# Performance work log

Measured on AMD Instinct MI355X. Metric: run time of the kernel, lower is better.

Reference implementation:

```python
import jax, jax.numpy as jnp
import numpy as np

N_NODES = 100000
N_EDGES = 1600000
IN_DIM, HID_DIM, OUT_DIM = 128, 64, 40


def gcn_conv(x, src, dst, deg_inv_sqrt, W, b):
    # PyG GCNConv: out[dst] += norm(e) * (x @ W)[src] ; norm = d^-1/2[src]*d^-1/2[dst]
    h = x @ W                                   # [N, out]
    norm = deg_inv_sqrt[src] * deg_inv_sqrt[dst]  # [E]
    msgs = h[src] * norm[:, None]               # [E, out] gather
    out = jax.ops.segment_sum(msgs, dst, num_segments=x.shape[0])  # scatter-add
    return out + b


def setup_inputs() -> dict:
    key = jax.random.key(0)
    k1, k2, k3, k4, k5, k6 = jax.random.split(key, 6)
    x = jax.random.normal(k1, (N_NODES, IN_DIM), dtype=jnp.float32)
    edge_index = jax.random.randint(k2, (2, N_EDGES), 0, N_NODES, dtype=jnp.int64)
    # Glorot-style init for linear weights, zero bias (as in GCNConv defaults)
    W1 = jax.random.normal(k3, (IN_DIM, HID_DIM), dtype=jnp.float32) / np.sqrt(IN_DIM)
    b1 = jnp.zeros((HID_DIM,), dtype=jnp.float32)
    W2 = jax.random.normal(k4, (HID_DIM, OUT_DIM), dtype=jnp.float32) / np.sqrt(HID_DIM)
    b2 = jnp.zeros((OUT_DIM,), dtype=jnp.float32)
    return {"x": x, "edge_index": edge_index, "W1": W1, "b1": b1, "W2": W2, "b2": b2}


def reference(x, edge_index, W1, b1, W2, b2):
    N = x.shape[0]
    loop = jnp.arange(N, dtype=edge_index.dtype)
    src = jnp.concatenate([edge_index[0], loop])  # add self-loops
    dst = jnp.concatenate([edge_index[1], loop])
    # symmetric normalization: degree over destination (col) with unit edge weights
    deg = jax.ops.segment_sum(jnp.ones_like(dst, dtype=x.dtype), dst, num_segments=N)
    deg_inv_sqrt = jnp.where(deg > 0, jax.lax.rsqrt(deg), 0.0)

    h = jax.nn.relu(gcn_conv(x, src, dst, deg_inv_sqrt, W1, b1))
    h = gcn_conv(h, src, dst, deg_inv_sqrt, W2, b2)
    return jax.nn.log_softmax(h, axis=1)
```

## Files before the change

### kernel.cpp

```cpp
#include <hip/hip_runtime.h>
#include <hip/hip_bf16.h>
#include <math.h>

typedef long long i64;
typedef __attribute__((ext_vector_type(8))) short short8v;
typedef __attribute__((ext_vector_type(4))) float f32x4;

__device__ __forceinline__ float bfu(unsigned short u) {
    union { unsigned int i; float f; } v; v.i = ((unsigned)u) << 16; return v.f;
}
__device__ __forceinline__ unsigned short f2b(float f) {
    __hip_bfloat16 h = __float2bfloat16(f);
    return *reinterpret_cast<unsigned short*>(&h);
}

#define NPB_SHIFT 9
#define NPB 512
#define LCAP 16384
#define P1C 8192

__global__ void k_zeroB(int* __restrict__ bcnt, int B) {
    int t = threadIdx.x;
    if (t <= B) bcnt[t] = 0;
}

__global__ __launch_bounds__(256) void k_p1count(
    const int* __restrict__ dst, int E, int B, int* __restrict__ bcnt) {
    __shared__ int lb[256];
    int t = threadIdx.x;
    lb[t] = 0; __syncthreads();
    int cpb = (E + gridDim.x - 1) / gridDim.x;
    int s0 = blockIdx.x * cpb, s1 = min(E, s0 + cpb);
    for (int i = s0 + t; i < s1; i += 256)
        atomicAdd(&lb[dst[i] >> NPB_SHIFT], 1);
    __syncthreads();
    if (t < B && lb[t]) atomicAdd(&bcnt[t], lb[t]);
}

__global__ void k_scanB(const int* __restrict__ bcnt, int B, int E,
                        int* __restrict__ bstart, int* __restrict__ cursor) {
    __shared__ int s[256];
    int t = threadIdx.x;
    int v = (t < B) ? bcnt[t] : 0;
    s[t] = v; __syncthreads();
    for (int off = 1; off < 256; off <<= 1) {
        int u = (t >= off) ? s[t - off] : 0;
        __syncthreads();
        s[t] += u;
        __syncthreads();
    }
    int excl = s[t] - v;
    if (t < B) { bstart[t] = excl; cursor[t] = excl; }
    if (t == 0) bstart[B] = E;
}

__global__ __launch_bounds__(256) void k_p1place(
    const int* __restrict__ src, const int* __restrict__ dst, int E, int B,
    int* __restrict__ cursor, unsigned* __restrict__ pairs) {
    __shared__ unsigned ls_p[P1C];
    __shared__ unsigned char ls_b[P1C];
    __shared__ int lb[256];
    __shared__ int lbase[256];
    int t = threadIdx.x;
    int s0 = blockIdx.x * P1C, s1 = min(E, s0 + P1C), n = s1 - s0;
    lb[t] = 0; __syncthreads();
    for (int i = t; i < n; i += 256) {
        int d = dst[s0 + i];
        int s = src[s0 + i];
        int bkt = d >> NPB_SHIFT;
        ls_p[i] = (unsigned)s | ((unsigned)(d & (NPB - 1)) << 17);
        ls_b[i] = (unsigned char)bkt;
        atomicAdd(&lb[bkt], 1);
    }
    __syncthreads();
    if (t < B && lb[t]) lbase[t] = atomicAdd(&cursor[t], lb[t]);
    __syncthreads();
    lb[t] = 0; __syncthreads();
    for (int i = t; i < n; i += 256) {
        int bkt = ls_b[i];
        int slot = atomicAdd(&lb[bkt], 1);
        pairs[lbase[bkt] + slot] = ls_p[i];
    }
}

__global__ __launch_bounds__(512) void k_p2(
    const unsigned* __restrict__ pairs, const int* __restrict__ bstart,
    int* __restrict__ rowptr, float* __restrict__ dinv,
    int* __restrict__ col, int N, int E) {
    __shared__ int lcnt[NPB];
    __shared__ int lscan[NPB];
    __shared__ int lcol[LCAP];
    int b = blockIdx.x, t = threadIdx.x;
    int lo = b << NPB_SHIFT, hi = min(N, lo + NPB), nn = hi - lo;
    int e0 = bstart[b], e1 = bstart[b + 1];
    lcnt[t] = 0; __syncthreads();
    for (int i = e0 + t; i < e1; i += 512)
        atomicAdd(&lcnt[(int)(pairs[i] >> 17)], 1);
    __syncthreads();
    int myc = (t < nn) ? lcnt[t] : 0;
    lscan[t] = myc; __syncthreads();
    for (int off = 1; off < 512; off <<= 1) {
        int u = (t >= off) ? lscan[t - off] : 0;
        __syncthreads();
        lscan[t] += u;
        __syncthreads();
    }
    if (t < nn) {
        rowptr[lo + t] = e0 + lscan[t] - myc;
        dinv[lo + t] = rsqrtf((float)(myc + 1));
    }
    if (t == 0 && hi == N) rowptr[N] = E;
    __syncthreads();
    lscan[t] -= myc;
    lcnt[t] = 0;
    __syncthreads();
    for (int i = e0 + t; i < e1; i += 512) {
        unsigned p = pairs[i];
        int n = (int)(p >> 17);
        int slot = atomicAdd(&lcnt[n], 1);
        int idx = lscan[n] + slot;
        if (idx < LCAP) lcol[idx] = (int)(p & 0x1FFFFu);
    }
    __syncthreads();
    int cnt = e1 - e0;
    for (int i = t; i < cnt; i += 512) col[e0 + i] = lcol[i];
}


__global__ __launch_bounds__(256) void k_gemm1m(
    const float* __restrict__ X, const float* __restrict__ W,
    const float* __restrict__ dinv, unsigned short* __restrict__ out, int N) {
    __shared__ unsigned short Xs[128 * 128];
    __shared__ unsigned short Wt[64 * 128];
    int tid = threadIdx.x;
    int row0 = blockIdx.x << 7;

    for (int i = tid; i < 2048; i += 256) {
        float4 v = *(const float4*)(W + i * 4);
        int k = (i * 4) >> 6, n = (i * 4) & 63;
        int kb = k * 2;
        *(unsigned short*)((char*)Wt + (n + 0) * 256 + (kb ^ (((n + 0) & 7) << 4))) = f2b(v.x);
        *(unsigned short*)((char*)Wt + (n + 1) * 256 + (kb ^ (((n + 1) & 7) << 4))) = f2b(v.y);
        *(unsigned short*)((char*)Wt + (n + 2) * 256 + (kb ^ (((n + 2) & 7) << 4))) = f2b(v.z);
        *(unsigned short*)((char*)Wt + (n + 3) * 256 + (kb ^ (((n + 3) & 7) << 4))) = f2b(v.w);
    }
    for (int i = tid; i < 4096; i += 256) {
        int r = i >> 5, c4 = i & 31;
        int gr = row0 + r;
        float4 v = make_float4(0.f, 0.f, 0.f, 0.f);
        if (gr < N) v = *(const float4*)(X + (size_t)gr * 128 + c4 * 4);
        ushort4 h;
        h.x = f2b(v.x); h.y = f2b(v.y); h.z = f2b(v.z); h.w = f2b(v.w);
        *(ushort4*)((char*)Xs + r * 256 + ((c4 * 8) ^ ((r & 7) << 4))) = h;
    }
    __syncthreads();

    int wid = tid >> 6, lane = tid & 63;
    int l15 = lane & 15, lg = lane >> 4;
    int wrow = wid * 32;

    f32x4 acc[2][4];
    #pragma unroll
    for (int fr = 0; fr < 2; fr++)
        #pragma unroll
        for (int fc = 0; fc < 4; fc++) acc[fr][fc] = (f32x4){0.f, 0.f, 0.f, 0.f};

    #pragma unroll
    for (int ks = 0; ks < 4; ks++) {
        int kbyte = ks * 64 + lg * 16;
        int ra0 = wrow + l15, ra1 = wrow + 16 + l15;
        short8v a0 = *(short8v*)((char*)Xs + ra0 * 256 + (kbyte ^ ((ra0 & 7) << 4)));
        short8v a1 = *(short8v*)((char*)Xs + ra1 * 256 + (kbyte ^ ((ra1 & 7) << 4)));
        int swb = kbyte ^ ((l15 & 7) << 4);
        short8v b0 = *(short8v*)((char*)Wt + (l15) * 256 + swb);
        short8v b1 = *(short8v*)((char*)Wt + (16 + l15) * 256 + swb);
        short8v b2 = *(short8v*)((char*)Wt + (32 + l15) * 256 + swb);
        short8v b3 = *(short8v*)((char*)Wt + (48 + l15) * 256 + swb);
        acc[0][0] = __builtin_amdgcn_mfma_f32_16x16x32_bf16(a0, b0, acc[0][0], 0, 0, 0);
        acc[0][1] = __builtin_amdgcn_mfma_f32_16x16x32_bf16(a0, b1, acc[0][1], 0, 0, 0);
        acc[0][2] = __builtin_amdgcn_mfma_f32_16x16x32_bf16(a0, b2, acc[0][2], 0, 0, 0);
        acc[0][3] = __builtin_amdgcn_mfma_f32_16x16x32_bf16(a0, b3, acc[0][3], 0, 0, 0);
        acc[1][0] = __builtin_amdgcn_mfma_f32_16x16x32_bf16(a1, b0, acc[1][0], 0, 0, 0);
        acc[1][1] = __builtin_amdgcn_mfma_f32_16x16x32_bf16(a1, b1, acc[1][1], 0, 0, 0);
        acc[1][2] = __builtin_amdgcn_mfma_f32_16x16x32_bf16(a1, b2, acc[1][2], 0, 0, 0);
        acc[1][3] = __builtin_amdgcn_mfma_f32_16x16x32_bf16(a1, b3, acc[1][3], 0, 0, 0);
    }

    float dv[2][4];
    #pragma unroll
    for (int fr = 0; fr < 2; fr++)
        #pragma unroll
        for (int reg = 0; reg < 4; reg++) {
            int grow = row0 + wrow + fr * 16 + lg * 4 + reg;
            dv[fr][reg] = (grow < N) ? dinv[grow] : 0.f;
        }
    #pragma unroll
    for (int fr = 0; fr < 2; fr++)
        #pragma unroll
        for (int fc = 0; fc < 4; fc++)
            #pragma unroll
            for (int reg = 0; reg < 4; reg++) {
                int grow = row0 + wrow + fr * 16 + lg * 4 + reg;
                if (grow < N)
                    out[(size_t)grow * 64 + fc * 16 + l15] = f2b(acc[fr][fc][reg] * dv[fr][reg]);
            }
}


template<bool L1>
__global__ __launch_bounds__(256) void k_agg(
    const unsigned short* __restrict__ gsrc, const int* __restrict__ rowptr,
    const int* __restrict__ col, const float* __restrict__ dinv,
    const float* __restrict__ b1, unsigned short* __restrict__ gout, int N) {
    int gw = (int)((blockIdx.x * 256u + threadIdx.x) >> 6);
    int lane = threadIdx.x & 63;
    int li = lane & 31;
    int node = gw * 2 + (lane >> 5);
    bool valid = node < N;
    int r0 = 0, r1 = 0;
    if (valid) { r0 = rowptr[node]; r1 = rowptr[node + 1]; }
    size_t fo = (size_t)(li * 2);
    float s0 = 0.f, s1 = 0.f;
    if (valid) {
        ushort2 u = *(const ushort2*)(gsrc + (((size_t)node) << 6) + fo);
        s0 = bfu(u.x); s1 = bfu(u.y);
    }
    int e = r0;
    for (; e + 16 <= r1; e += 16) {
        int cc[16];
        #pragma unroll
        for (int j = 0; j < 16; j++) cc[j] = col[e + j];
        float va[16], vb[16];
        #pragma unroll
        for (int j = 0; j < 16; j++) {
            ushort2 u = *(const ushort2*)(gsrc + (((size_t)cc[j]) << 6) + fo);
            va[j] = bfu(u.x); vb[j] = bfu(u.y);
        }
        #pragma unroll
        for (int s = 1; s < 16; s <<= 1)
            #pragma unroll
            for (int j = 0; j < 16; j += 2 * s) { va[j] += va[j + s]; vb[j] += vb[j + s]; }
        s0 += va[0]; s1 += vb[0];
    }
    for (; e + 4 <= r1; e += 4) {
        int c0 = col[e], c1 = col[e + 1], c2 = col[e + 2], c3 = col[e + 3];
        ushort2 u0 = *(const ushort2*)(gsrc + (((size_t)c0) << 6) + fo);
        ushort2 u1 = *(const ushort2*)(gsrc + (((size_t)c1) << 6) + fo);
        ushort2 u2 = *(const ushort2*)(gsrc + (((size_t)c2) << 6) + fo);
        ushort2 u3 = *(const ushort2*)(gsrc + (((size_t)c3) << 6) + fo);
        s0 += (bfu(u0.x) + bfu(u1.x)) + (bfu(u2.x) + bfu(u3.x));
        s1 += (bfu(u0.y) + bfu(u1.y)) + (bfu(u2.y) + bfu(u3.y));
    }
    for (; e < r1; ++e) {
        ushort2 u = *(const ushort2*)(gsrc + (((size_t)col[e]) << 6) + fo);
        s0 += bfu(u.x); s1 += bfu(u.y);
    }
    if (valid) {
        float dvn = dinv[node];
        float o0, o1;
        if (L1) {
            o0 = dvn * fmaxf(dvn * s0 + b1[li * 2 + 0], 0.f);
            o1 = dvn * fmaxf(dvn * s1 + b1[li * 2 + 1], 0.f);
        } else {
            o0 = dvn * s0;
            o1 = dvn * s1;
        }
        ushort2 w;
        w.x = f2b(o0); w.y = f2b(o1);
        *(ushort2*)(gout + (((size_t)node) << 6) + fo) = w;
    }
}


__global__ __launch_bounds__(256) void k_gemm2s(
    const unsigned short* __restrict__ t, const float* __restrict__ W2,
    const float* __restrict__ b2, float* __restrict__ out, int N) {
    __shared__ unsigned short Xs[256 * 72];
    __shared__ float W2s[64 * 40];
    __shared__ float b2s[40];
    int tid = threadIdx.x;
    int row0 = blockIdx.x * 256;
    for (int i = tid; i < 640; i += 256)
        ((float4*)W2s)[i] = ((const float4*)W2)[i];
    if (tid < 40) b2s[tid] = b2[tid];
    for (int c = tid; c < 2048; c += 256) {
        int r = c >> 3, j = c & 7;
        int gr = row0 + r;
        uint4 v = make_uint4(0u, 0u, 0u, 0u);
        if (gr < N) v = *(const uint4*)(t + (((size_t)gr) << 6) + j * 8);
        *(uint4*)(Xs + r * 72 + j * 8) = v;
    }
    __syncthreads();
    int row = row0 + tid;
    if (row >= N) return;
    float acc[40];
    #pragma unroll
    for (int c = 0; c < 40; c++) acc[c] = b2s[c];
    const unsigned short* xr = Xs + tid * 72;
    for (int k = 0; k < 64; k++) {
        float x = bfu(xr[k]);
        #pragma unroll
        for (int j = 0; j < 10; j++) {
            float4 w = ((const float4*)(W2s + k * 40))[j];
            acc[4 * j + 0] += x * w.x;
            acc[4 * j + 1] += x * w.y;
            acc[4 * j + 2] += x * w.z;
            acc[4 * j + 3] += x * w.w;
        }
    }
    float m = acc[0];
    #pragma unroll
    for (int c = 1; c < 40; c++) m = fmaxf(m, acc[c]);
    float p = 0.f;
    #pragma unroll
    for (int c = 0; c < 40; c++) p += __expf(acc[c] - m);
    float l = __logf(p) + m;
    float* orow = out + (size_t)row * 40;
    #pragma unroll
    for (int j = 0; j < 10; j++) {
        float4 ov;
        ov.x = acc[4 * j + 0] - l;
        ov.y = acc[4 * j + 1] - l;
        ov.z = acc[4 * j + 2] - l;
        ov.w = acc[4 * j + 3] - l;
        *(float4*)(orow + 4 * j) = ov;
    }
}


extern "C" void kernel_launch(void* const* d_in, const int* in_sizes, int n_in,
                              void* d_out, int out_size, void* d_ws, size_t ws_size,
                              hipStream_t stream) {
    const float* x  = (const float*)d_in[0];
    const int*   ei = (const int*)d_in[1];
    const float* W1 = (const float*)d_in[2];
    const float* b1 = (const float*)d_in[3];
    const float* W2 = (const float*)d_in[4];
    const float* b2 = (const float*)d_in[5];
    float* out = (float*)d_out;

    const int N = in_sizes[0] / 128;
    const int E = in_sizes[1] / 2;
    const int B = (N + NPB - 1) >> NPB_SHIFT;
    const int* src = ei;
    const int* dst = ei + E;

    char* w = (char*)d_ws;
    size_t off = 0;
    auto alloc = [&](size_t bytes) -> char* {
        char* p = w + off;
        off += (bytes + 255) & ~(size_t)255;
        return p;
    };
    int*   bcnt   = (int*)alloc((size_t)(B + 1) * 4);
    int*   bstart = (int*)alloc((size_t)(B + 1) * 4);
    int*   cursor = (int*)alloc((size_t)B * 4);
    int*   rowptr = (int*)alloc((size_t)(N + 1) * 4);
    float* dinv   = (float*)alloc((size_t)N * 4);
    int*   col    = (int*)alloc((size_t)E * 4 + 256);
    size_t shbytes = (size_t)E * 4 > (size_t)N * 64 * 2 ? (size_t)E * 4 : (size_t)N * 64 * 2;
    char*  sh     = alloc(shbytes);
    unsigned short* q = (unsigned short*)alloc((size_t)N * 64 * 2);
    unsigned* pairs  = (unsigned*)sh;
    unsigned short* g1 = (unsigned short*)sh;
    unsigned short* t  = (unsigned short*)sh;

    k_zeroB<<<1, 256, 0, stream>>>(bcnt, B);
    k_p1count<<<256, 256, 0, stream>>>(dst, E, B, bcnt);
    k_scanB<<<1, 256, 0, stream>>>(bcnt, B, E, bstart, cursor);
    int nch = (E + P1C - 1) / P1C;
    k_p1place<<<nch, 256, 0, stream>>>(src, dst, E, B, cursor, pairs);
    k_p2<<<B, 512, 0, stream>>>(pairs, bstart, rowptr, dinv, col, N, E);

    int nwaves = (N + 1) / 2;
    int aggblocks = (nwaves + 3) / 4;

    k_gemm1m<<<(N + 127) / 128, 256, 0, stream>>>(x, W1, dinv, g1, N);
    k_agg<true><<<aggblocks, 256, 0, stream>>>(g1, rowptr, col, dinv, b1, q, N);

    k_agg<false><<<aggblocks, 256, 0, stream>>>(q, rowptr, col, dinv, b1, t, N);
    k_gemm2s<<<(N + 255) / 256, 256, 0, stream>>>(t, W2, b2, out, N);
}
```

Before: 182.0 us.

## Fuse second aggregation with W2 GEMM and log_softmax

Replaces the second aggregation kernel and the separate W2 GEMM plus log_softmax kernel with one fused kernel. Each block aggregates 8 nodes into shared memory, then 32 lanes per node compute the 40 outputs and a shuffle-based log_softmax. This removes one launch and the global write and re-read of the intermediate bf16 features. In exchange, each small block reloads W2 into shared memory and adds a block barrier, which adds cache traffic.

```diff
diff --git a/kernel.cpp b/kernel.cpp
--- a/kernel.cpp
+++ b/kernel.cpp
@@ -207,8 +207,7 @@
 }
 
 
-template<bool L1>
-__global__ __launch_bounds__(256) void k_agg(
+__global__ __launch_bounds__(256) void k_aggL1(
     const unsigned short* __restrict__ gsrc, const int* __restrict__ rowptr,
     const int* __restrict__ col, const float* __restrict__ dinv,
     const float* __restrict__ b1, unsigned short* __restrict__ gout, int N) {
@@ -257,14 +256,8 @@
     }
     if (valid) {
         float dvn = dinv[node];
-        float o0, o1;
-        if (L1) {
-            o0 = dvn * fmaxf(dvn * s0 + b1[li * 2 + 0], 0.f);
-            o1 = dvn * fmaxf(dvn * s1 + b1[li * 2 + 1], 0.f);
-        } else {
-            o0 = dvn * s0;
-            o1 = dvn * s1;
-        }
+        float o0 = dvn * fmaxf(dvn * s0 + b1[li * 2 + 0], 0.f);
+        float o1 = dvn * fmaxf(dvn * s1 + b1[li * 2 + 1], 0.f);
         ushort2 w;
         w.x = f2b(o0); w.y = f2b(o1);
         *(ushort2*)(gout + (((size_t)node) << 6) + fo) = w;
@@ -272,58 +265,89 @@
 }
 
 
-__global__ __launch_bounds__(256) void k_gemm2s(
-    const unsigned short* __restrict__ t, const float* __restrict__ W2,
-    const float* __restrict__ b2, float* __restrict__ out, int N) {
-    __shared__ unsigned short Xs[256 * 72];
+__global__ __launch_bounds__(256) void k_agg2f(
+    const unsigned short* __restrict__ gsrc, const int* __restrict__ rowptr,
+    const int* __restrict__ col, const float* __restrict__ dinv,
+    const float* __restrict__ W2, const float* __restrict__ b2,
+    float* __restrict__ out, int N) {
+    __shared__ float trow[8][64];
     __shared__ float W2s[64 * 40];
     __shared__ float b2s[40];
     int tid = threadIdx.x;
-    int row0 = blockIdx.x * 256;
-    for (int i = tid; i < 640; i += 256)
-        ((float4*)W2s)[i] = ((const float4*)W2)[i];
+    for (int idx = tid; idx < 2560; idx += 256) W2s[idx] = W2[idx];
     if (tid < 40) b2s[tid] = b2[tid];
-    for (int c = tid; c < 2048; c += 256) {
-        int r = c >> 3, j = c & 7;
-        int gr = row0 + r;
-        uint4 v = make_uint4(0u, 0u, 0u, 0u);
-        if (gr < N) v = *(const uint4*)(t + (((size_t)gr) << 6) + j * 8);
-        *(uint4*)(Xs + r * 72 + j * 8) = v;
-    }
-    __syncthreads();
-    int row = row0 + tid;
-    if (row >= N) return;
-    float acc[40];
-    #pragma unroll
-    for (int c = 0; c < 40; c++) acc[c] = b2s[c];
-    const unsigned short* xr = Xs + tid * 72;
+
+    int lane = tid & 63;
+    int li = lane & 31;
+    int g = (tid >> 6) * 2 + (lane >> 5);
+    int node = blockIdx.x * 8 + g;
+    bool valid = node < N;
+    int r0 = 0, r1 = 0;
+    if (valid) { r0 = rowptr[node]; r1 = rowptr[node + 1]; }
+    size_t fo = (size_t)(li * 2);
+    float s0 = 0.f, s1 = 0.f;
+    if (valid) {
+        ushort2 u = *(const ushort2*)(gsrc + (((size_t)node) << 6) + fo);
+        s0 = bfu(u.x); s1 = bfu(u.y);
+    }
+    int e = r0;
+    for (; e + 16 <= r1; e += 16) {
+        int cc[16];
+        #pragma unroll
+        for (int j = 0; j < 16; j++) cc[j] = col[e + j];
+        float va[16], vb[16];
+        #pragma unroll
+        for (int j = 0; j < 16; j++) {
+            ushort2 u = *(const ushort2*)(gsrc + (((size_t)cc[j]) << 6) + fo);
+            va[j] = bfu(u.x); vb[j] = bfu(u.y);
+        }
+        #pragma unroll
+        for (int s = 1; s < 16; s <<= 1)
+            #pragma unroll
+            for (int j = 0; j < 16; j += 2 * s) { va[j] += va[j + s]; vb[j] += vb[j + s]; }
+        s0 += va[0]; s1 += vb[0];
+    }
+    for (; e + 4 <= r1; e += 4) {
+        int c0 = col[e], c1 = col[e + 1], c2 = col[e + 2], c3 = col[e + 3];
+        ushort2 u0 = *(const ushort2*)(gsrc + (((size_t)c0) << 6) + fo);
+        ushort2 u1 = *(const ushort2*)(gsrc + (((size_t)c1) << 6) + fo);
+        ushort2 u2 = *(const ushort2*)(gsrc + (((size_t)c2) << 6) + fo);
+        ushort2 u3 = *(const ushort2*)(gsrc + (((size_t)c3) << 6) + fo);
+        s0 += (bfu(u0.x) + bfu(u1.x)) + (bfu(u2.x) + bfu(u3.x));
+        s1 += (bfu(u0.y) + bfu(u1.y)) + (bfu(u2.y) + bfu(u3.y));
+    }
+    for (; e < r1; ++e) {
+        ushort2 u = *(const ushort2*)(gsrc + (((size_t)col[e]) << 6) + fo);
+        s0 += bfu(u.x); s1 += bfu(u.y);
+    }
+    float dvn = valid ? dinv[node] : 0.f;
+    trow[g][li * 2 + 0] = dvn * s0;
+    trow[g][li * 2 + 1] = dvn * s1;
+    __syncthreads();
+
+    int g2 = tid >> 5;
+    int c = tid & 31;
+    int c1 = 32 + (c & 7);
+    int node2 = blockIdx.x * 8 + g2;
+    float acc0 = b2s[c], acc1 = b2s[c1];
+    const float* tr = trow[g2];
+    #pragma unroll 8
     for (int k = 0; k < 64; k++) {
-        float x = bfu(xr[k]);
-        #pragma unroll
-        for (int j = 0; j < 10; j++) {
-            float4 w = ((const float4*)(W2s + k * 40))[j];
-            acc[4 * j + 0] += x * w.x;
-            acc[4 * j + 1] += x * w.y;
-            acc[4 * j + 2] += x * w.z;
-            acc[4 * j + 3] += x * w.w;
-        }
-    }
-    float m = acc[0];
-    #pragma unroll
-    for (int c = 1; c < 40; c++) m = fmaxf(m, acc[c]);
-    float p = 0.f;
-    #pragma unroll
-    for (int c = 0; c < 40; c++) p += __expf(acc[c] - m);
+        float xv = tr[k];
+        acc0 += xv * W2s[k * 40 + c];
+        acc1 += xv * W2s[k * 40 + c1];
+    }
+    bool c2v = (c < 8);
+    float m = fmaxf(acc0, c2v ? acc1 : -INFINITY);
+    #pragma unroll
+    for (int off = 16; off > 0; off >>= 1) m = fmaxf(m, __shfl_xor(m, off, 32));
+    float p = __expf(acc0 - m) + (c2v ? __expf(acc1 - m) : 0.f);
+    #pragma unroll
+    for (int off = 16; off > 0; off >>= 1) p += __shfl_xor(p, off, 32);
     float l = __logf(p) + m;
-    float* orow = out + (size_t)row * 40;
-    #pragma unroll
-    for (int j = 0; j < 10; j++) {
-        float4 ov;
-        ov.x = acc[4 * j + 0] - l;
-        ov.y = acc[4 * j + 1] - l;
-        ov.z = acc[4 * j + 2] - l;
-        ov.w = acc[4 * j + 3] - l;
-        *(float4*)(orow + 4 * j) = ov;
+    if (node2 < N) {
+        out[(size_t)node2 * 40 + c] = acc0 - l;
+        if (c2v) out[(size_t)node2 * 40 + c1] = acc1 - l;
     }
 }
 
@@ -363,7 +387,6 @@
     unsigned short* q = (unsigned short*)alloc((size_t)N * 64 * 2);
     unsigned* pairs  = (unsigned*)sh;
     unsigned short* g1 = (unsigned short*)sh;
-    unsigned short* t  = (unsigned short*)sh;
 
     k_zeroB<<<1, 256, 0, stream>>>(bcnt, B);
     k_p1count<<<256, 256, 0, stream>>>(dst, E, B, bcnt);
@@ -372,12 +395,10 @@
     k_p1place<<<nch, 256, 0, stream>>>(src, dst, E, B, cursor, pairs);
     k_p2<<<B, 512, 0, stream>>>(pairs, bstart, rowptr, dinv, col, N, E);
 
-    int nwaves = (N + 1) / 2;
-    int aggblocks = (nwaves + 3) / 4;
+    int aggblocks = (N + 7) / 8;
 
     k_gemm1m<<<(N + 127) / 128, 256, 0, stream>>>(x, W1, dinv, g1, N);
-    k_agg<true><<<aggblocks, 256, 0, stream>>>(g1, rowptr, col, dinv, b1, q, N);
-
-    k_agg<false><<<aggblocks, 256, 0, stream>>>(q, rowptr, col, dinv, b1, t, N);
-    k_gemm2s<<<(N + 255) / 256, 256, 0, stream>>>(t, W2, b2, out, N);
-}
+    k_aggL1<<<aggblocks, 256, 0, stream>>>(g1, rowptr, col, dinv, b1, q, N);
+
+    k_agg2f<<<aggblocks, 256, 0, stream>>>(q, rowptr, col, dinv, W2, b2, out, N);
+}
```

After: 193.2 us. 6.1% more time.
